# Kernel tuning notes

Hardware: AMD Instinct MI355X
Metric: run time of the kernel (lower is better)

The kernel has to match this reference:

```python
import jax, jax.numpy as jnp
import numpy as np

B, N, F_IN, K, OUT = 64, 512, 6, 8, 3
SLOPE = 0.01  # torch LeakyReLU default negative_slope


def lrelu(x):
    return jnp.where(x >= 0, x, SLOPE * x)


def edge_mlp(e, w1, b1, w2, b2):
    # Linear -> LeakyReLU -> Linear -> LeakyReLU (EdgeConvMLP / mlp1)
    return lrelu(lrelu(e @ w1 + b1) @ w2 + b2)


def dyn_edge_conv(x, w1, b1, w2, b2):
    # x: [B, N, F]. kNN in feature space within each graph (self included,
    # matching torch_cluster.knn used by PyG DynamicEdgeConv).
    x2 = jnp.sum(x * x, -1)                                   # [B, N]
    d = x2[:, :, None] + x2[:, None, :] - 2.0 * jnp.einsum('bnf,bmf->bnm', x, x)
    idx = jax.lax.top_k(-d, K)[1]                              # [B, N, K]
    xj = jax.vmap(lambda xb, ib: xb[ib])(x, idx)               # [B, N, K, F]
    xi = jnp.broadcast_to(x[:, :, None, :], xj.shape)
    e = jnp.concatenate([xi, xj - xi], -1)                     # [B, N, K, 2F]
    h = edge_mlp(e, w1, b1, w2, b2)                            # [B, N, K, 256]
    return h.max(axis=2)                                       # max aggregation


def _lin(key, din, dout):
    kw, kb = jax.random.split(key)
    s = 1.0 / np.sqrt(din)
    w = jax.random.uniform(kw, (din, dout), jnp.float32, -s, s)
    b = jax.random.uniform(kb, (dout,), jnp.float32, -s, s)
    return w, b


def setup_inputs() -> dict:
    key = jax.random.key(0)
    ks = jax.random.split(key, 20)
    inp = {}
    inp['x'] = jax.random.normal(ks[0], (B * N, F_IN), jnp.float32)
    inp['edge_index'] = jax.random.randint(ks[1], (2, B * N * K), 0, B * N, jnp.int64)  # unused
    inp['batch'] = jnp.repeat(jnp.arange(B, dtype=jnp.int64), N)
    dims = [(2 * F_IN, 336, 256), (512, 336, 256), (512, 336, 256), (512, 336, 256)]
    for i, (din, dh, do) in enumerate(dims):
        w1, b1 = _lin(ks[2 + 2 * i], din, dh)
        w2, b2 = _lin(ks[3 + 2 * i], dh, do)
        inp[f'c{i+1}_w1'], inp[f'c{i+1}_b1'] = w1, b1
        inp[f'c{i+1}_w2'], inp[f'c{i+1}_b2'] = w2, b2
    inp['m1_w1'], inp['m1_b1'] = _lin(ks[10], 256 * 4 + F_IN, 336)
    inp['m1_w2'], inp['m1_b2'] = _lin(ks[11], 336, 256)
    inp['m2_w1'], inp['m2_b1'] = _lin(ks[12], 256, 128)
    inp['m2_w2'], inp['m2_b2'] = _lin(ks[13], 128, OUT)
    return inp


def reference(x, edge_index, batch,
              c1_w1, c1_b1, c1_w2, c1_b2,
              c2_w1, c2_b1, c2_w2, c2_b2,
              c3_w1, c3_b1, c3_w2, c3_b2,
              c4_w1, c4_b1, c4_w2, c4_b2,
              m1_w1, m1_b1, m1_w2, m1_b2,
              m2_w1, m2_b1, m2_w2, m2_b2):
    # edge_index is unused: DynamicEdgeConv rebuilds the kNN graph each layer.
    # Equal-sized graphs: reshape instead of segment ops (batch = repeat(arange(B), N)).
    xb = x.reshape(B, N, F_IN)
    x1 = dyn_edge_conv(xb, c1_w1, c1_b1, c1_w2, c1_b2)
    x2 = dyn_edge_conv(x1, c2_w1, c2_b1, c2_w2, c2_b2)
    x3 = dyn_edge_conv(x2, c3_w1, c3_b1, c3_w2, c3_b2)
    x4 = dyn_edge_conv(x3, c4_w1, c4_b1, c4_w2, c4_b2)
    h = jnp.concatenate([xb, x1, x2, x3, x4], -1)   # [B, N, 1030]
    h = edge_mlp(h, m1_w1, m1_b1, m1_w2, m1_b2)     # [B, N, 256]
    g = h.mean(axis=1)                              # global_mean_pool -> [B, 256]
    return lrelu(g @ m2_w1 + m2_b1) @ m2_w2 + m2_b2  # [B, OUT]
```

## Files before the change

### kernel.cpp

```cpp
#include <hip/hip_runtime.h>
#include <hip/hip_bf16.h>


#define DEVFN __device__ __forceinline__
DEVFN float lrelu(float v) { return fmaxf(v, 0.01f * v); }

using bf16x8 = __attribute__((ext_vector_type(8))) short;
using f32x4  = __attribute__((ext_vector_type(4))) float;

template<int N> struct IC { static constexpr int value = N; };

DEVFN unsigned short f2bf(float v) {
    __hip_bfloat16 h = __float2bfloat16(v);
    return *(unsigned short*)&h;
}
DEVFN float bf2f(unsigned short u) {
    return __uint_as_float((unsigned)u << 16);
}

struct PDesc { const float* src; unsigned short* dst; int Kt, NT, N, mode, p0, p1, Ksrc; };
struct PTable { PDesc d[13]; };

__global__ __launch_bounds__(256) void pack_kernel(PTable tb) {
    PDesc d = tb.d[blockIdx.y];
    int i = blockIdx.x * 256 + threadIdx.x;
    int tot = d.Kt * d.NT * 512;
    if (i >= tot) return;
    int j = i & 7, lane = (i >> 3) & 63;
    int tile = i >> 9;
    int nt = tile % d.NT, kt = tile / d.NT;
    int k = kt * 32 + ((lane >> 4) << 3) + j;
    int n = nt * 16 + (lane & 15);
    float v = 0.f;
    if (d.mode == 0) {
        if (k < d.Ksrc) v = d.src[(size_t)k * d.N + n];
    } else if (d.mode == 1) {
        if (k < d.p1) v = d.src[(size_t)k * d.N + n] - d.src[(size_t)(k + d.p1) * d.N + n];
        else if (k >= d.p0 && k < d.p0 + d.p1) v = d.src[(size_t)(k - d.p0 + d.p1) * d.N + n];
    } else if (d.mode == 2) {
        if (k < 6) v = d.src[(size_t)k * d.N + n];
        else if (k >= 32 && k < 1056) v = d.src[(size_t)(k - 26) * d.N + n];
    } else {
        v = d.src[(size_t)(k + d.p0) * d.N + n];
    }
    d.dst[i] = f2bf(v);
}

__global__ __launch_bounds__(256) void xbprep_kernel(const float* __restrict__ xb,
                                                     unsigned short* __restrict__ xcat,
                                                     float* __restrict__ g) {
    int p = blockIdx.x * 256 + threadIdx.x;
    if (p >= 32768) return;
    if (p < 16384) g[p] = 0.f;
    unsigned short r[16];
    #pragma unroll
    for (int c = 0; c < 6; ++c) r[c] = f2bf(xb[p * 6 + c]);
    #pragma unroll
    for (int c = 6; c < 16; ++c) r[c] = 0;
    unsigned short* xc = xcat + (size_t)p * 1056;
    #pragma unroll
    for (int c = 0; c < 16; ++c) xc[c] = r[c];
    #pragma unroll
    for (int c = 16; c < 32; ++c) xc[c] = 0;
}

template<int F>
__global__ __launch_bounds__(256) void norms_kernel(const float* __restrict__ f,
                                                    float* __restrict__ nrm) {
    int p = blockIdx.x * 256 + threadIdx.x;
    if (p >= 64 * 512) return;
    const float* r = f + (size_t)p * F;
    float s = 0.f;
    #pragma unroll
    for (int i = 0; i < F; ++i) s += r[i] * r[i];
    nrm[p] = s;
}

template<int F>
__global__ __launch_bounds__(256) void knn_kernel(const float* __restrict__ feat,
                                                  const float* __restrict__ nrm,
                                                  int* __restrict__ knn) {
    constexpr int FP = (F == 6) ? 8 : (F + 4);
    __shared__ float Xq[32 * FP];
    __shared__ float Xc[32 * FP];
    __shared__ float qn[32], cn[32];
    __shared__ float dt[32 * 33];
    const int t  = threadIdx.x;
    const int b  = blockIdx.x >> 4;
    const int n0 = (blockIdx.x & 15) << 5;
    const float* fg = feat + (size_t)b * 512 * F;

    for (int i = t; i < 32 * F; i += 256) {
        int r = i / F, c = i - r * F;
        Xq[r * FP + c] = fg[(size_t)(n0 + r) * F + c];
    }
    if (t < 32) qn[t] = nrm[b * 512 + n0 + t];

    float d8[8]; int i8[8];
    #pragma unroll
    for (int k = 0; k < 8; ++k) { d8[k] = 3.4e38f; i8[k] = 0; }

    const int q = t >> 3, cs = t & 7;

    for (int ct = 0; ct < 16; ++ct) {
        const int c0 = ct << 5;
        __syncthreads();
        for (int i = t; i < 32 * F; i += 256) {
            int r = i / F, c = i - r * F;
            Xc[r * FP + c] = fg[(size_t)(c0 + r) * F + c];
        }
        if (t < 32) cn[t] = nrm[b * 512 + c0 + t];
        __syncthreads();

        float acc[4] = {0.f, 0.f, 0.f, 0.f};
        #pragma unroll
        for (int f = 0; f < F; ++f) {
            float qv = Xq[q * FP + f];
            #pragma unroll
            for (int j = 0; j < 4; ++j) acc[j] += qv * Xc[(cs + 8 * j) * FP + f];
        }
        #pragma unroll
        for (int j = 0; j < 4; ++j)
            dt[q * 33 + cs + 8 * j] = qn[q] + cn[cs + 8 * j] - 2.f * acc[j];
        __syncthreads();

        if (t < 32) {
            #pragma unroll 1
            for (int i = 0; i < 32; ++i) {
                float d = dt[t * 33 + i];
                if (d < d8[7]) {
                    d8[7] = d; i8[7] = c0 + i;
                    #pragma unroll
                    for (int s = 7; s >= 1; --s) {
                        if (d8[s] < d8[s - 1]) {
                            float td = d8[s]; d8[s] = d8[s - 1]; d8[s - 1] = td;
                            int   ti = i8[s]; i8[s] = i8[s - 1]; i8[s - 1] = ti;
                        }
                    }
                }
            }
        }
    }
    if (t < 32) {
        #pragma unroll
        for (int k = 0; k < 8; ++k)
            knn[((size_t)b * 512 + n0 + t) * 8 + k] = i8[k];
    }
}

__global__ __launch_bounds__(256, 2)
void knn_mfma(const unsigned short* __restrict__ xfl,
              const float* __restrict__ nrm,
              int* __restrict__ knn) {
    __shared__ unsigned short Ch[64 * 72], Cl[64 * 72];
    __shared__ float dt[64 * 66];
    __shared__ float qn[64], cn[64];
    float* mD = dt;
    int*   mI = (int*)(dt + 2048);

    const int t  = threadIdx.x;
    const int l  = t & 63, w = t >> 6;
    const int m16 = l & 15, q4 = l >> 4;
    const int bx = blockIdx.x;
    const int slot = bx >> 3;
    const int b  = (bx & 7) + 8 * (slot >> 3);
    const int qs = (slot & 7) << 6;

    if (t < 64) qn[t] = nrm[b * 512 + qs + t];

    bf16x8 qh[4][2], ql[4][2];
    {
        const unsigned short* qr = xfl + (size_t)(b * 512 + qs + w * 16 + m16) * 512;
        #pragma unroll
        for (int kc = 0; kc < 4; ++kc)
            #pragma unroll
            for (int kt = 0; kt < 2; ++kt) {
                qh[kc][kt] = *(const bf16x8*)(qr + kc * 64 + kt * 32 + q4 * 8);
                ql[kc][kt] = *(const bf16x8*)(qr + 256 + kc * 64 + kt * 32 + q4 * 8);
            }
    }

    float d8[8]; int i8[8];
    #pragma unroll
    for (int k = 0; k < 8; ++k) { d8[k] = 3.4e38f; i8[k] = 0x7fffffff; }

    const int sr = t >> 2;
    const int sc = (t & 3) << 4;
    const int tq = t & 63, sub = t >> 6;

    for (int cs = 0; cs < 8; ++cs) {
        const int c0 = cs << 6;
        if (t < 64) cn[t] = nrm[b * 512 + c0 + t];

        f32x4 acc[4];
        #pragma unroll
        for (int i = 0; i < 4; ++i) acc[i] = (f32x4){0.f, 0.f, 0.f, 0.f};

        #pragma unroll
        for (int kc = 0; kc < 4; ++kc) {
            const int k0 = kc << 6;
            __syncthreads();
            {
                const unsigned short* cr = xfl + (size_t)(b * 512 + c0 + sr) * 512;
                *(uint4*)&Ch[sr * 72 + sc]     = *(const uint4*)(cr + k0 + sc);
                *(uint4*)&Ch[sr * 72 + sc + 8] = *(const uint4*)(cr + k0 + sc + 8);
                *(uint4*)&Cl[sr * 72 + sc]     = *(const uint4*)(cr + 256 + k0 + sc);
                *(uint4*)&Cl[sr * 72 + sc + 8] = *(const uint4*)(cr + 256 + k0 + sc + 8);
            }
            __syncthreads();

            #pragma unroll
            for (int kt = 0; kt < 2; ++kt) {
                const int ko = kt * 32 + q4 * 8;
                bf16x8 ah = qh[kc][kt];
                bf16x8 al = ql[kc][kt];
                #pragma unroll
                for (int nt = 0; nt < 4; ++nt) {
                    bf16x8 bh = *(const bf16x8*)&Ch[(nt * 16 + m16) * 72 + ko];
                    bf16x8 bl = *(const bf16x8*)&Cl[(nt * 16 + m16) * 72 + ko];
                    acc[nt] = __builtin_amdgcn_mfma_f32_16x16x32_bf16(ah, bh, acc[nt], 0, 0, 0);
                    acc[nt] = __builtin_amdgcn_mfma_f32_16x16x32_bf16(ah, bl, acc[nt], 0, 0, 0);
                    acc[nt] = __builtin_amdgcn_mfma_f32_16x16x32_bf16(al, bh, acc[nt], 0, 0, 0);
                }
            }
        }

        #pragma unroll
        for (int nt = 0; nt < 4; ++nt) {
            float cv = cn[nt * 16 + m16];
            #pragma unroll
            for (int rr = 0; rr < 4; ++rr) {
                int qr = w * 16 + q4 * 4 + rr;
                dt[qr * 66 + nt * 16 + m16] = qn[qr] + cv - 2.f * acc[nt][rr];
            }
        }
        __syncthreads();

        {
            const float* drow = &dt[tq * 66 + sub * 16];
            #pragma unroll 1
            for (int j = 0; j < 16; ++j) {
                float d = drow[j];
                if (d < d8[7]) {
                    d8[7] = d; i8[7] = c0 + sub * 16 + j;
                    #pragma unroll
                    for (int s = 7; s >= 1; --s) {
                        if (d8[s] < d8[s - 1]) {
                            float td = d8[s]; d8[s] = d8[s - 1]; d8[s - 1] = td;
                            int   ti = i8[s]; i8[s] = i8[s - 1]; i8[s - 1] = ti;
                        }
                    }
                }
            }
        }
        __syncthreads();
    }

    #pragma unroll
    for (int k = 0; k < 8; ++k) {
        mD[(tq * 4 + sub) * 8 + k] = d8[k];
        mI[(tq * 4 + sub) * 8 + k] = i8[k];
    }
    __syncthreads();
    if (t < 64) {
        int p[4] = {0, 0, 0, 0};
        int outb = (b * 512 + qs + t) * 8;
        #pragma unroll 1
        for (int k = 0; k < 8; ++k) {
            float bd = 3.5e38f; int bi = 0x7fffffff; int bs = 0;
            #pragma unroll
            for (int s = 0; s < 4; ++s) {
                if (p[s] < 8) {
                    float dd = mD[(t * 4 + s) * 8 + p[s]];
                    int   ii = mI[(t * 4 + s) * 8 + p[s]];
                    if (dd < bd || (dd == bd && ii < bi)) { bd = dd; bi = ii; bs = s; }
                }
            }
            knn[outb + k] = bi;
            p[bs]++;
        }
    }
}

__global__ __launch_bounds__(256)
void pgemm1_kernel(const float* __restrict__ xb,
                   const float* __restrict__ W1,
                   const float* __restrict__ B1,
                   unsigned short* __restrict__ Pa,
                   unsigned short* __restrict__ Pb) {
    int i = blockIdx.x * 256 + threadIdx.x;
    if (i >= 32768 * 42) return;
    int p = i / 42, c8 = i - p * 42;
    int c0 = c8 * 8;
    float x[6];
    #pragma unroll
    for (int k = 0; k < 6; ++k) x[k] = xb[p * 6 + k];
    float sa[8], sb[8];
    #pragma unroll
    for (int j = 0; j < 8; ++j) { sa[j] = B1[c0 + j]; sb[j] = 0.f; }
    #pragma unroll
    for (int k = 0; k < 6; ++k) {
        const float* wra = W1 + (size_t)k * 336 + c0;
        const float* wrb = W1 + (size_t)(k + 6) * 336 + c0;
        #pragma unroll
        for (int j = 0; j < 8; ++j) {
            float wb = wrb[j];
            sa[j] += x[k] * (wra[j] - wb);
            sb[j] += x[k] * wb;
        }
    }
    unsigned short oa[8], ob[8];
    #pragma unroll
    for (int j = 0; j < 8; ++j) { oa[j] = f2bf(sa[j]); ob[j] = f2bf(sb[j]); }
    *(uint4*)&Pa[(size_t)p * 336 + c0] = *(uint4*)oa;
    *(uint4*)&Pb[(size_t)p * 336 + c0] = *(uint4*)ob;
}

__global__ __launch_bounds__(256, 3)
void pgemm_kernel(const unsigned short* __restrict__ xfl,
                  const unsigned short* __restrict__ Wa,
                  const unsigned short* __restrict__ Wb,
                  const float* __restrict__ B1,
                  unsigned short* __restrict__ Pa,
                  unsigned short* __restrict__ Pb) {
    __shared__ unsigned short smem[64 * 344];
    const int t = threadIdx.x;
    const int l = t & 63, w = t >> 6;
    const int q4 = l >> 4, m16 = l & 15;
    const int s1 = w * 6;
    const int bx = blockIdx.x & 511;
    const bool isA = !(blockIdx.x & 512);
    const unsigned short* W1ap = isA ? Wa : Wb;
    unsigned short*       Pp   = isA ? Pa : Pb;
    const int slot = bx >> 3;
    const int r0 = ((bx & 7) + 8 * (slot >> 3)) * 512 + (slot & 7) * 64;

    {
        const int r = t >> 2;
        const unsigned short* srow = xfl + (size_t)(r0 + r) * 512;
        #pragma unroll
        for (int s = 0; s < 8; ++s) {
            int c16 = (t & 3) + (s << 2);
            *(uint4*)&smem[r * 264 + c16 * 8] = *(const uint4*)(srow + c16 * 8);
        }
    }
    __syncthreads();

    f32x4 acc[4][6];
    #pragma unroll
    for (int mt = 0; mt < 4; ++mt)
        #pragma unroll
        for (int n = 0; n < 6; ++n) acc[mt][n] = (f32x4){0.f, 0.f, 0.f, 0.f};

    auto run = [&](auto c1c) {
        constexpr int C1 = decltype(c1c)::value;
        bf16x8 bcur[C1];
        {
            const unsigned short* bp = W1ap + ((size_t)s1 * 64 + l) * 8;
            #pragma unroll
            for (int n = 0; n < C1; ++n) bcur[n] = *(const bf16x8*)(bp + n * 512);
        }
        #pragma unroll 1
        for (int kt = 0; kt < 8; ++kt) {
            bf16x8 bnext[C1];
            if (kt + 1 < 8) {
                const unsigned short* bp = W1ap + ((size_t)((kt + 1) * 21 + s1) * 64 + l) * 8;
                #pragma unroll
                for (int n = 0; n < C1; ++n) bnext[n] = *(const bf16x8*)(bp + n * 512);
            }
            bf16x8 af[4];
            #pragma unroll
            for (int mt = 0; mt < 4; ++mt)
                af[mt] = *(const bf16x8*)&smem[(mt * 16 + m16) * 264 + q4 * 8 + kt * 32];
            #pragma unroll
            for (int n = 0; n < C1; ++n)
                #pragma unroll
                for (int mt = 0; mt < 4; ++mt)
                    acc[mt][n] = __builtin_amdgcn_mfma_f32_16x16x32_bf16(af[mt], bcur[n], acc[mt][n], 0, 0, 0);
            #pragma unroll
            for (int n = 0; n < C1; ++n) bcur[n] = bnext[n];
        }
    };
    if (w < 3) run(IC<6>{});
    else       run(IC<3>{});

    __syncthreads();
    {
        const int c1 = (w < 3) ? 6 : 3;
        for (int n = 0; n < c1; ++n) {
            int col = (s1 + n) * 16 + m16;
            float bias = isA ? B1[col] : 0.f;
            #pragma unroll
            for (int mt = 0; mt < 4; ++mt)
                #pragma unroll
                for (int r = 0; r < 4; ++r)
                    smem[(mt * 16 + q4 * 4 + r) * 344 + col] = f2bf(acc[mt][n][r] + bias);
        }
    }
    __syncthreads();
    {
        uint4* dst = (uint4*)(Pp + (size_t)r0 * 336);
        const uint4* src = (const uint4*)smem;
        #pragma unroll 1
        for (int i = t; i < 2688; i += 256)
            dst[i] = src[(i / 42) * 43 + (i % 42)];
    }
}

template<int MODE>
__global__ __launch_bounds__(256, MODE == 3 ? 4 : 3)
void mfma_mlp(const unsigned short* __restrict__ featbf,
              const int* __restrict__ knn,
              const unsigned short* __restrict__ W1p, const float* __restrict__ B1,
              const unsigned short* __restrict__ W2p, const float* __restrict__ B2,
              const unsigned short* __restrict__ Pp,
              const unsigned short* __restrict__ Pbp,
              float* __restrict__ outf,
              unsigned short* __restrict__ xcat, int sliceoff,
              unsigned short* __restrict__ xfl, float* __restrict__ nrm) {
    constexpr int ROWS = 32;

    __shared__ unsigned short smem[ROWS * 360];
    __shared__ int rowi[32];
    __shared__ int rowj[32];
    __shared__ float nparts[4][4];

    const int t = threadIdx.x;
    const int l = t & 63, w = t >> 6;
    const int q4 = l >> 4, m16 = l & 15;
    const int s1 = w * 6;
    const int s2 = w * 4;

    const int bx = blockIdx.x;
    int p0;
    if constexpr (MODE == 3) {
        int slot = bx >> 3;
        int g = (bx & 7) + 8 * (slot >> 7);
        p0 = g * 512 + (slot & 127) * 4;
    } else {
        int slot = bx >> 3;
        int g = (bx & 7) + 8 * (slot >> 4);
        p0 = g * 512 + (slot & 15) * 32;
    }

    if constexpr (MODE == 3) {
        if (t < 32) {
            int pt = p0 + (t >> 3);
            rowi[t] = pt;
            rowj[t] = (pt & ~511) + knn[pt * 8 + (t & 7)];
        }
        __syncthreads();
        const int row = t >> 3;
        const int u0  = t & 7;
        const unsigned short* va = Pp  + (size_t)rowi[row] * 336;
        const unsigned short* vb = Pbp + (size_t)rowj[row] * 336;
        uint4 A[6], Bv[6];
        #pragma unroll
        for (int k = 0; k < 6; ++k) {
            int u = u0 + 8 * k;
            if (u < 42) {
                A[k]  = *(const uint4*)(va + u * 8);
                Bv[k] = *(const uint4*)(vb + u * 8);
            }
        }
        #pragma unroll
        for (int k = 0; k < 6; ++k) {
            int u = u0 + 8 * k;
            if (u < 42) {
                const unsigned* ua = (const unsigned*)&A[k];
                const unsigned* ub = (const unsigned*)&Bv[k];
                uint4 ov;
                unsigned short* o = (unsigned short*)&ov;
                #pragma unroll
                for (int j = 0; j < 4; ++j) {
                    unsigned va_ = ua[j], vb_ = ub[j];
                    float slo = __uint_as_float(va_ << 16) + __uint_as_float(vb_ << 16);
                    float shi = __uint_as_float(va_ & 0xffff0000u) + __uint_as_float(vb_ & 0xffff0000u);
                    o[2 * j]     = f2bf(lrelu(slo));
                    o[2 * j + 1] = f2bf(lrelu(shi));
                }
                *(uint4*)&smem[row * 360 + u * 8] = ov;
            }
        }
    } else {
        f32x4 acc1[2][6];
        #pragma unroll
        for (int mt = 0; mt < 2; ++mt)
            #pragma unroll
            for (int n = 0; n < 6; ++n) acc1[mt][n] = (f32x4){0.f, 0.f, 0.f, 0.f};

        auto g1 = [&](auto c1c, int ktbase) {
            constexpr int C1 = decltype(c1c)::value;
            bf16x8 bcur[C1];
            {
                const unsigned short* bp =
                    W1p + ((size_t)(ktbase * 21 + s1) * 64 + l) * 8;
                #pragma unroll
                for (int n = 0; n < C1; ++n) bcur[n] = *(const bf16x8*)(bp + n * 512);
            }
            #pragma unroll 1
            for (int kt = 0; kt < 11; ++kt) {
                bf16x8 bnext[C1];
                if (kt + 1 < 11) {
                    const unsigned short* bp =
                        W1p + ((size_t)((ktbase + kt + 1) * 21 + s1) * 64 + l) * 8;
                    #pragma unroll
                    for (int n = 0; n < C1; ++n) bnext[n] = *(const bf16x8*)(bp + n * 512);
                }
                bf16x8 af[2];
                #pragma unroll
                for (int mt = 0; mt < 2; ++mt)
                    af[mt] = *(const bf16x8*)&smem[(mt * 16 + m16) * 360 + q4 * 8 + kt * 32];
                #pragma unroll
                for (int n = 0; n < C1; ++n)
                    #pragma unroll
                    for (int mt = 0; mt < 2; ++mt)
                        acc1[mt][n] = __builtin_amdgcn_mfma_f32_16x16x32_bf16(af[mt], bcur[n], acc1[mt][n], 0, 0, 0);
                #pragma unroll
                for (int n = 0; n < C1; ++n) bcur[n] = bnext[n];
            }
        };

        for (int kc = 0; kc < 3; ++kc) {
            __syncthreads();
            {
                const int r = t >> 3, tc = t & 7;
                const unsigned short* srow =
                    featbf + (size_t)(p0 + r) * 1056 + kc * 352;
                #pragma unroll
                for (int s = 0; s < 6; ++s) {
                    int c16 = tc + (s << 3);
                    if (c16 < 44)
                        *(uint4*)&smem[r * 360 + c16 * 8] = *(const uint4*)(srow + c16 * 8);
                }
            }
            __syncthreads();

            if (w < 3) g1(IC<6>{}, kc * 11);
            else       g1(IC<3>{}, kc * 11);
        }
        __syncthreads();

        {
            const int c1 = (w < 3) ? 6 : 3;
            for (int n = 0; n < c1; ++n) {
                int nt = s1 + n;
                float b = B1[nt * 16 + m16];
                #pragma unroll
                for (int mt = 0; mt < 2; ++mt) {
                    #pragma unroll
                    for (int r = 0; r < 4; ++r) {
                        int row = mt * 16 + q4 * 4 + r;
                        float v = acc1[mt][n][r] + b;
                        smem[row * 360 + nt * 16 + m16] = f2bf(lrelu(v));
                    }
                }
            }
        }
    }

    if (t < ROWS) {
        #pragma unroll
        for (int c = 336; c < 352; ++c) smem[t * 360 + c] = 0;
    }
    __syncthreads();

    f32x4 acc2[2][4];
    #pragma unroll
    for (int mt = 0; mt < 2; ++mt)
        #pragma unroll
        for (int n = 0; n < 4; ++n) acc2[mt][n] = (f32x4){0.f, 0.f, 0.f, 0.f};
    {
        bf16x8 b0[4], b1f[4];
        {
            const unsigned short* bp0 = W2p + ((size_t)s2 * 64 + l) * 8;
            const unsigned short* bp1 = W2p + ((size_t)(16 + s2) * 64 + l) * 8;
            #pragma unroll
            for (int n = 0; n < 4; ++n) {
                b0[n]  = *(const bf16x8*)(bp0 + n * 512);
                b1f[n] = *(const bf16x8*)(bp1 + n * 512);
            }
        }
        #pragma unroll 1
        for (int kt = 0; kt < 11; ++kt) {
            bf16x8 b2[4];
            if (kt + 2 < 11) {
                const unsigned short* bp = W2p + ((size_t)((kt + 2) * 16 + s2) * 64 + l) * 8;
                #pragma unroll
                for (int n = 0; n < 4; ++n) b2[n] = *(const bf16x8*)(bp + n * 512);
            }
            bf16x8 af[2];
            #pragma unroll
            for (int mt = 0; mt < 2; ++mt)
                af[mt] = *(const bf16x8*)&smem[(mt * 16 + m16) * 360 + q4 * 8 + kt * 32];
            #pragma unroll
            for (int n = 0; n < 4; ++n)
                #pragma unroll
                for (int mt = 0; mt < 2; ++mt)
                    acc2[mt][n] = __builtin_amdgcn_mfma_f32_16x16x32_bf16(af[mt], b0[n], acc2[mt][n], 0, 0, 0);
            #pragma unroll
            for (int n = 0; n < 4; ++n) { b0[n] = b1f[n]; b1f[n] = b2[n]; }
        }
    }

    if constexpr (MODE == 3) {
        __syncthreads();
        unsigned short* sh = smem;
        #pragma unroll
        for (int mt = 0; mt < 2; ++mt) {
            float nsum = 0.f;
            int plocal = mt * 2 + (q4 >> 1);
            #pragma unroll
            for (int n = 0; n < 4; ++n) {
                int nt = s2 + n;
                float b = B2[nt * 16 + m16];
                float mv = -3.4e38f;
                #pragma unroll
                for (int r = 0; r < 4; ++r) mv = fmaxf(mv, lrelu(acc2[mt][n][r] + b));
                mv = fmaxf(mv, __shfl_xor(mv, 16, 64));
                if ((q4 & 1) == 0) {
                    int col = nt * 16 + m16;
                    unsigned short hi = f2bf(mv);
                    float fhi = bf2f(hi);
                    unsigned short lo = f2bf(mv - fhi);
                    float xr = fhi + bf2f(lo);
                    nsum += xr * xr;
                    sh[plocal * 512 + col] = hi;
                    sh[plocal * 512 + 256 + col] = lo;
                }
            }
            #pragma unroll
            for (int o = 1; o < 16; o <<= 1) nsum += __shfl_xor(nsum, o, 64);
            if ((q4 & 1) == 0 && m16 == 0) nparts[plocal][w] = nsum;
        }
        __syncthreads();
        {
            int r = t >> 6, cb = (t & 63) * 8;
            int p = p0 + r;
            uint4 v0 = *(uint4*)&sh[r * 512 + cb];
            *(uint4*)&xfl[(size_t)p * 512 + cb] = v0;
            if (cb < 256)
                *(uint4*)&xcat[(size_t)p * 1056 + sliceoff + cb] = v0;
        }
        if (t < 4)
            nrm[p0 + t] =
                nparts[t][0] + nparts[t][1] + nparts[t][2] + nparts[t][3];
    } else {
        const int bgraph = p0 >> 9;
        #pragma unroll
        for (int n = 0; n < 4; ++n) {
            int nt = s2 + n;
            float b = B2[nt * 16 + m16];
            float s = 0.f;
            #pragma unroll
            for (int mt = 0; mt < 2; ++mt)
                #pragma unroll
                for (int r = 0; r < 4; ++r)
                    s += lrelu(acc2[mt][n][r] + b);
            s += __shfl_xor(s, 16, 64);
            s += __shfl_xor(s, 32, 64);
            if (q4 == 0)
                atomicAdd(outf + bgraph * 256 + nt * 16 + m16, s * (1.f / 512.f));
        }
    }
}

__global__ __launch_bounds__(128) void head_kernel(const float* __restrict__ g,
                                                   const float* __restrict__ w1,
                                                   const float* __restrict__ b1,
                                                   const float* __restrict__ w2,
                                                   const float* __restrict__ b2,
                                                   float* __restrict__ out) {
    __shared__ float gs[256];
    __shared__ float hid[128];
    int b = blockIdx.x, t = threadIdx.x;
    gs[t] = g[b * 256 + t];
    gs[t + 128] = g[b * 256 + t + 128];
    __syncthreads();
    float s = b1[t];
    for (int c = 0; c < 256; ++c) s += gs[c] * w1[c * 128 + t];
    hid[t] = lrelu(s);
    __syncthreads();
    if (t < 3) {
        float o = b2[t];
        for (int j = 0; j < 128; ++j) o += hid[j] * w2[j * 3 + t];
        out[b * 3 + t] = o;
    }
}

extern "C" void kernel_launch(void* const* d_in, const int* in_sizes, int n_in,
                              void* d_out, int out_size, void* d_ws, size_t ws_size,
                              hipStream_t stream) {
    const float* xb = (const float*)d_in[0];
    const float* c_w1[4] = { (const float*)d_in[3],  (const float*)d_in[7],
                             (const float*)d_in[11], (const float*)d_in[15] };
    const float* c_b1[4] = { (const float*)d_in[4],  (const float*)d_in[8],
                             (const float*)d_in[12], (const float*)d_in[16] };
    const float* c_w2[4] = { (const float*)d_in[5],  (const float*)d_in[9],
                             (const float*)d_in[13], (const float*)d_in[17] };
    const float* c_b2[4] = { (const float*)d_in[6],  (const float*)d_in[10],
                             (const float*)d_in[14], (const float*)d_in[18] };
    const float* m1w1 = (const float*)d_in[19];
    const float* m1b1 = (const float*)d_in[20];
    const float* m1w2 = (const float*)d_in[21];
    const float* m1b2 = (const float*)d_in[22];
    const float* m2w1 = (const float*)d_in[23];
    const float* m2b1 = (const float*)d_in[24];
    const float* m2w2 = (const float*)d_in[25];
    const float* m2b2 = (const float*)d_in[26];

    char* base = (char*)d_ws;
    size_t off = 0;
    auto alloc = [&](size_t bytes) { char* p = base + off; off = (off + bytes + 255) & ~(size_t)255; return p; };
    int*            knn   = (int*)           alloc((size_t)32768 * 8 * 4);
    float*          nrm   = (float*)         alloc((size_t)32768 * 4);
    char*           Preg  =                  alloc((size_t)32768 * 256 * 4);
    unsigned short* Ppb   = (unsigned short*)alloc((size_t)32768 * 336 * 2);
    float*          g     = (float*)         alloc(64 * 256 * 4);
    unsigned short* xcat  = (unsigned short*)alloc((size_t)32768 * 1056 * 2);
    unsigned short* xfl   = (unsigned short*)alloc((size_t)32768 * 512 * 2);
    unsigned short* w1p1  = (unsigned short*)alloc((size_t)1  * 21 * 512 * 2);
    unsigned short* w2p1  = (unsigned short*)alloc((size_t)11 * 16 * 512 * 2);
    unsigned short* w1a[3]; unsigned short* w1b[3]; unsigned short* w2p[3];
    for (int i = 0; i < 3; ++i) {
        w1a[i] = (unsigned short*)alloc((size_t)8  * 21 * 512 * 2);
        w1b[i] = (unsigned short*)alloc((size_t)8  * 21 * 512 * 2);
        w2p[i] = (unsigned short*)alloc((size_t)11 * 16 * 512 * 2);
    }
    unsigned short* m1p1  = (unsigned short*)alloc((size_t)33 * 21 * 512 * 2);
    unsigned short* m1p2  = (unsigned short*)alloc((size_t)11 * 16 * 512 * 2);
    unsigned short* Pp = (unsigned short*)Preg;

    PTable tb;
    tb.d[0] = { c_w1[0], w1p1, 1,  21, 336, 1, 16,  6,   0   };
    tb.d[1] = { c_w2[0], w2p1, 11, 16, 256, 0, 0,   0,   336 };
    for (int i = 0; i < 3; ++i) {
        tb.d[2 + 3 * i] = { c_w1[i + 1], w1a[i], 8,  21, 336, 1, 0,   256, 0   };
        tb.d[3 + 3 * i] = { c_w1[i + 1], w1b[i], 8,  21, 336, 3, 256, 0,   0   };
        tb.d[4 + 3 * i] = { c_w2[i + 1], w2p[i], 11, 16, 256, 0, 0,   0,   336 };
    }
    tb.d[11] = { m1w1, m1p1, 33, 21, 336, 2, 0, 0, 0   };
    tb.d[12] = { m1w2, m1p2, 11, 16, 256, 0, 0, 0, 336 };
    pack_kernel<<<dim3(1386, 13), dim3(256), 0, stream>>>(tb);
    xbprep_kernel<<<128, 256, 0, stream>>>(xb, xcat, g);

    norms_kernel<6><<<128, 256, 0, stream>>>(xb, nrm);
    knn_kernel<6><<<1024, 256, 0, stream>>>(xb, nrm, knn);
    pgemm1_kernel<<<5376, 256, 0, stream>>>(xb, c_w1[0], c_b1[0], Pp, Ppb);
    mfma_mlp<3><<<8192, 256, 0, stream>>>(nullptr, knn,
                                          nullptr, nullptr, w2p1, c_b2[0], Pp, Ppb,
                                          nullptr, xcat, 32, xfl, nrm);

    for (int l = 1; l < 4; ++l) {
        int dstslice = 32 + l * 256;
        knn_mfma<<<512, 256, 0, stream>>>(xfl, nrm, knn);
        pgemm_kernel<<<1024, 256, 0, stream>>>(xfl, w1a[l - 1], w1b[l - 1], c_b1[l], Pp, Ppb);
        mfma_mlp<3><<<8192, 256, 0, stream>>>(nullptr, knn,
                                              nullptr, nullptr, w2p[l - 1], c_b2[l], Pp, Ppb,
                                              nullptr, xcat, dstslice, xfl, nrm);
    }

    mfma_mlp<2><<<1024, 256, 0, stream>>>(xcat, nullptr,
                                          m1p1, m1b1, m1p2, m1b2, nullptr, nullptr,
                                          g, nullptr, 0, nullptr, nullptr);

    head_kernel<<<64, 128, 0, stream>>>(g, m2w1, m2b1, m2w2, m2b2, (float*)d_out);
}
```

Measured before the change: 956.5 us.

## Merge kNN and P-GEMM into one heterogeneous launch, raise MLP occupancy bounds

Combines the per-layer kNN MFMA kernel and the P projection GEMM into one kernel that interleaves block roles (one kNN block per two GEMM blocks) over a shared LDS buffer. Both read only xfl and are independent, so they can run concurrently and fill the GPU better, with one fewer launch. The fused kernel uses a launch bound of 2 blocks, which may cap pgemm occupancy below its old 3. Separately, the mfma_mlp launch bounds rise from 4/3 to 6/4 blocks per CU, which pressures registers and risks spills.

```diff
diff --git a/kernel.cpp b/kernel.cpp
--- a/kernel.cpp
+++ b/kernel.cpp
@@ -148,20 +148,21 @@
     }
 }
 
-__global__ __launch_bounds__(256, 2)
-void knn_mfma(const unsigned short* __restrict__ xfl,
-              const float* __restrict__ nrm,
-              int* __restrict__ knn) {
-    __shared__ unsigned short Ch[64 * 72], Cl[64 * 72];
-    __shared__ float dt[64 * 66];
-    __shared__ float qn[64], cn[64];
+__device__ void knn_mfma_body(int bx, char* sm,
+                              const unsigned short* __restrict__ xfl,
+                              const float* __restrict__ nrm,
+                              int* __restrict__ knn) {
+    unsigned short* Ch = (unsigned short*)sm;
+    unsigned short* Cl = Ch + 4608;
+    float* dt = (float*)(sm + 18432);
+    float* qn = (float*)(sm + 35328);
+    float* cn = (float*)(sm + 35584);
     float* mD = dt;
     int*   mI = (int*)(dt + 2048);
 
     const int t  = threadIdx.x;
     const int l  = t & 63, w = t >> 6;
     const int m16 = l & 15, q4 = l >> 4;
-    const int bx = blockIdx.x;
     const int slot = bx >> 3;
     const int b  = (bx & 7) + 8 * (slot >> 3);
     const int qs = (slot & 7) << 6;
@@ -282,6 +283,113 @@
     }
 }
 
+__device__ void pgemm_body(int bx, char* sm,
+                           const unsigned short* __restrict__ xfl,
+                           const unsigned short* __restrict__ Wa,
+                           const unsigned short* __restrict__ Wb,
+                           const float* __restrict__ B1,
+                           unsigned short* __restrict__ Pa,
+                           unsigned short* __restrict__ Pb) {
+    unsigned short* smem = (unsigned short*)sm;
+    const int t = threadIdx.x;
+    const int l = t & 63, w = t >> 6;
+    const int q4 = l >> 4, m16 = l & 15;
+    const int s1 = w * 6;
+    const int bi = bx & 511;
+    const bool isA = !(bx & 512);
+    const unsigned short* W1ap = isA ? Wa : Wb;
+    unsigned short*       Pp   = isA ? Pa : Pb;
+    const int slot = bi >> 3;
+    const int r0 = ((bi & 7) + 8 * (slot >> 3)) * 512 + (slot & 7) * 64;
+
+    {
+        const int r = t >> 2;
+        const unsigned short* srow = xfl + (size_t)(r0 + r) * 512;
+        #pragma unroll
+        for (int s = 0; s < 8; ++s) {
+            int c16 = (t & 3) + (s << 2);
+            *(uint4*)&smem[r * 264 + c16 * 8] = *(const uint4*)(srow + c16 * 8);
+        }
+    }
+    __syncthreads();
+
+    f32x4 acc[4][6];
+    #pragma unroll
+    for (int mt = 0; mt < 4; ++mt)
+        #pragma unroll
+        for (int n = 0; n < 6; ++n) acc[mt][n] = (f32x4){0.f, 0.f, 0.f, 0.f};
+
+    auto run = [&](auto c1c) {
+        constexpr int C1 = decltype(c1c)::value;
+        bf16x8 bcur[C1];
+        {
+            const unsigned short* bp = W1ap + ((size_t)s1 * 64 + l) * 8;
+            #pragma unroll
+            for (int n = 0; n < C1; ++n) bcur[n] = *(const bf16x8*)(bp + n * 512);
+        }
+        #pragma unroll 1
+        for (int kt = 0; kt < 8; ++kt) {
+            bf16x8 bnext[C1];
+            if (kt + 1 < 8) {
+                const unsigned short* bp = W1ap + ((size_t)((kt + 1) * 21 + s1) * 64 + l) * 8;
+                #pragma unroll
+                for (int n = 0; n < C1; ++n) bnext[n] = *(const bf16x8*)(bp + n * 512);
+            }
+            bf16x8 af[4];
+            #pragma unroll
+            for (int mt = 0; mt < 4; ++mt)
+                af[mt] = *(const bf16x8*)&smem[(mt * 16 + m16) * 264 + q4 * 8 + kt * 32];
+            #pragma unroll
+            for (int n = 0; n < C1; ++n)
+                #pragma unroll
+                for (int mt = 0; mt < 4; ++mt)
+                    acc[mt][n] = __builtin_amdgcn_mfma_f32_16x16x32_bf16(af[mt], bcur[n], acc[mt][n], 0, 0, 0);
+            #pragma unroll
+            for (int n = 0; n < C1; ++n) bcur[n] = bnext[n];
+        }
+    };
+    if (w < 3) run(IC<6>{});
+    else       run(IC<3>{});
+
+    __syncthreads();
+    {
+        const int c1 = (w < 3) ? 6 : 3;
+        for (int n = 0; n < c1; ++n) {
+            int col = (s1 + n) * 16 + m16;
+            float bias = isA ? B1[col] : 0.f;
+            #pragma unroll
+            for (int mt = 0; mt < 4; ++mt)
+                #pragma unroll
+                for (int r = 0; r < 4; ++r)
+                    smem[(mt * 16 + q4 * 4 + r) * 344 + col] = f2bf(acc[mt][n][r] + bias);
+        }
+    }
+    __syncthreads();
+    {
+        uint4* dst = (uint4*)(Pp + (size_t)r0 * 336);
+        const uint4* src = (const uint4*)smem;
+        #pragma unroll 1
+        for (int i = t; i < 2688; i += 256)
+            dst[i] = src[(i / 42) * 43 + (i % 42)];
+    }
+}
+
+__global__ __launch_bounds__(256, 2)
+void knn_pgemm(const unsigned short* __restrict__ xfl,
+               const float* __restrict__ nrm,
+               int* __restrict__ knn,
+               const unsigned short* __restrict__ Wa,
+               const unsigned short* __restrict__ Wb,
+               const float* __restrict__ B1,
+               unsigned short* __restrict__ Pa,
+               unsigned short* __restrict__ Pb) {
+    __shared__ char sm[64 * 344 * 2];
+    const int bx = blockIdx.x;
+    const int r3 = bx % 3;
+    if (r3 == 0) knn_mfma_body(bx / 3, sm, xfl, nrm, knn);
+    else         pgemm_body(2 * (bx / 3) + r3 - 1, sm, xfl, Wa, Wb, B1, Pa, Pb);
+}
+
 __global__ __launch_bounds__(256)
 void pgemm1_kernel(const float* __restrict__ xb,
                    const float* __restrict__ W1,
@@ -316,99 +424,8 @@
     *(uint4*)&Pb[(size_t)p * 336 + c0] = *(uint4*)ob;
 }
 
-__global__ __launch_bounds__(256, 3)
-void pgemm_kernel(const unsigned short* __restrict__ xfl,
-                  const unsigned short* __restrict__ Wa,
-                  const unsigned short* __restrict__ Wb,
-                  const float* __restrict__ B1,
-                  unsigned short* __restrict__ Pa,
-                  unsigned short* __restrict__ Pb) {
-    __shared__ unsigned short smem[64 * 344];
-    const int t = threadIdx.x;
-    const int l = t & 63, w = t >> 6;
-    const int q4 = l >> 4, m16 = l & 15;
-    const int s1 = w * 6;
-    const int bx = blockIdx.x & 511;
-    const bool isA = !(blockIdx.x & 512);
-    const unsigned short* W1ap = isA ? Wa : Wb;
-    unsigned short*       Pp   = isA ? Pa : Pb;
-    const int slot = bx >> 3;
-    const int r0 = ((bx & 7) + 8 * (slot >> 3)) * 512 + (slot & 7) * 64;
-
-    {
-        const int r = t >> 2;
-        const unsigned short* srow = xfl + (size_t)(r0 + r) * 512;
-        #pragma unroll
-        for (int s = 0; s < 8; ++s) {
-            int c16 = (t & 3) + (s << 2);
-            *(uint4*)&smem[r * 264 + c16 * 8] = *(const uint4*)(srow + c16 * 8);
-        }
-    }
-    __syncthreads();
-
-    f32x4 acc[4][6];
-    #pragma unroll
-    for (int mt = 0; mt < 4; ++mt)
-        #pragma unroll
-        for (int n = 0; n < 6; ++n) acc[mt][n] = (f32x4){0.f, 0.f, 0.f, 0.f};
-
-    auto run = [&](auto c1c) {
-        constexpr int C1 = decltype(c1c)::value;
-        bf16x8 bcur[C1];
-        {
-            const unsigned short* bp = W1ap + ((size_t)s1 * 64 + l) * 8;
-            #pragma unroll
-            for (int n = 0; n < C1; ++n) bcur[n] = *(const bf16x8*)(bp + n * 512);
-        }
-        #pragma unroll 1
-        for (int kt = 0; kt < 8; ++kt) {
-            bf16x8 bnext[C1];
-            if (kt + 1 < 8) {
-                const unsigned short* bp = W1ap + ((size_t)((kt + 1) * 21 + s1) * 64 + l) * 8;
-                #pragma unroll
-                for (int n = 0; n < C1; ++n) bnext[n] = *(const bf16x8*)(bp + n * 512);
-            }
-            bf16x8 af[4];
-            #pragma unroll
-            for (int mt = 0; mt < 4; ++mt)
-                af[mt] = *(const bf16x8*)&smem[(mt * 16 + m16) * 264 + q4 * 8 + kt * 32];
-            #pragma unroll
-            for (int n = 0; n < C1; ++n)
-                #pragma unroll
-                for (int mt = 0; mt < 4; ++mt)
-                    acc[mt][n] = __builtin_amdgcn_mfma_f32_16x16x32_bf16(af[mt], bcur[n], acc[mt][n], 0, 0, 0);
-            #pragma unroll
-            for (int n = 0; n < C1; ++n) bcur[n] = bnext[n];
-        }
-    };
-    if (w < 3) run(IC<6>{});
-    else       run(IC<3>{});
-
-    __syncthreads();
-    {
-        const int c1 = (w < 3) ? 6 : 3;
-        for (int n = 0; n < c1; ++n) {
-            int col = (s1 + n) * 16 + m16;
-            float bias = isA ? B1[col] : 0.f;
-            #pragma unroll
-            for (int mt = 0; mt < 4; ++mt)
-                #pragma unroll
-                for (int r = 0; r < 4; ++r)
-                    smem[(mt * 16 + q4 * 4 + r) * 344 + col] = f2bf(acc[mt][n][r] + bias);
-        }
-    }
-    __syncthreads();
-    {
-        uint4* dst = (uint4*)(Pp + (size_t)r0 * 336);
-        const uint4* src = (const uint4*)smem;
-        #pragma unroll 1
-        for (int i = t; i < 2688; i += 256)
-            dst[i] = src[(i / 42) * 43 + (i % 42)];
-    }
-}
-
 template<int MODE>
-__global__ __launch_bounds__(256, MODE == 3 ? 4 : 3)
+__global__ __launch_bounds__(256, MODE == 3 ? 6 : 4)
 void mfma_mlp(const unsigned short* __restrict__ featbf,
               const int* __restrict__ knn,
               const unsigned short* __restrict__ W1p, const float* __restrict__ B1,
@@ -753,8 +770,8 @@
 
     for (int l = 1; l < 4; ++l) {
         int dstslice = 32 + l * 256;
-        knn_mfma<<<512, 256, 0, stream>>>(xfl, nrm, knn);
-        pgemm_kernel<<<1024, 256, 0, stream>>>(xfl, w1a[l - 1], w1b[l - 1], c_b1[l], Pp, Ppb);
+        knn_pgemm<<<1536, 256, 0, stream>>>(xfl, nrm, knn,
+                                            w1a[l - 1], w1b[l - 1], c_b1[l], Pp, Ppb);
         mfma_mlp<3><<<8192, 256, 0, stream>>>(nullptr, knn,
                                               nullptr, nullptr, w2p[l - 1], c_b2[l], Pp, Ppb,
                                               nullptr, xcat, dstslice, xfl, nrm);
```

After: 2.011 ms. +110.3%, slower.
